# Kernel optimization log

Measured on AMD Instinct MI355X. Metric: run time of the kernel, lower is better.

Reference implementation:

```python
import jax, jax.numpy as jnp
import numpy as np

EPS = 1e-06
S = 0.025
ALPHA = 0.98
DELTA = 2.0
R = 0.5


def setup_inputs() -> dict:
    key = jax.random.key(0)
    # mel spectrogram magnitudes: non-negative
    x = jax.random.uniform(key, (32, 8192, 128), dtype=jnp.float32)
    return {"x": x}


def reference(x):
    # EMA smoother over time: M[0] = x[0]; M[t] = (1-s)*M[t-1] + s*x[t]
    # x: [B, T, F] -> scan over time with carry [B, F]
    def step(m_prev, x_t):
        m = (1.0 - S) * m_prev + S * x_t
        return m, m

    x_t_major = jnp.moveaxis(x[:, 1:, :], 1, 0)  # [T-1, B, F]
    _, ms = jax.lax.scan(step, x[:, 0, :], x_t_major)  # ms: [T-1, B, F]
    M = jnp.concatenate([x[:, :1, :], jnp.moveaxis(ms, 0, 1)], axis=1)  # [B, T, F]

    # PCEN: (x / (M + eps)^alpha + delta)^r - delta^r
    out = (x / jnp.power(M + EPS, ALPHA) + DELTA) ** R - DELTA ** R
    return out
```

## Files before the change

### kernel.cpp

```cpp
#include <hip/hip_runtime.h>
#include <math.h>


#define BB 32
#define TT 8192
#define FF 128
#define KK 64
#define CC (TT / KK)
#define WW 256
#define AA 0.975f
#define SS 0.025f

__device__ __forceinline__ float pcen_out(float xv, float m) {
    float mp = m + 1e-6f;
    float p = __builtin_amdgcn_exp2f(-0.98f * __builtin_amdgcn_logf(mp));
    return sqrtf(fmaf(xv, p, 2.0f)) - 1.41421356237309505f;
}

__global__ __launch_bounds__(128) void pcen_kernel(const float* __restrict__ x,
                                                   float* __restrict__ out) {
    const int job = blockIdx.x;
    const int b   = job >> 6;
    const int k   = job & (KK - 1);
    const int f   = threadIdx.x;
    const int t0  = k * CC;

    const size_t base = ((size_t)b * TT + t0) * FF + f;
    const float* xp = x + base;
    float*       op = out + base;

    float m;
    if (k == 0) {
        float xv = xp[0];
        m = xv;
        __builtin_nontemporal_store(pcen_out(xv, m), op);
    } else {
        const int w = (t0 < WW) ? t0 : WW;
        const float* wp = xp - (size_t)w * FF;
        m = wp[0];
        #pragma unroll 8
        for (int j = 1; j < w; ++j) {
            m = fmaf(AA, m, SS * wp[(size_t)j * FF]);
        }
        float xv = xp[0];
        m = fmaf(AA, m, SS * xv);
        __builtin_nontemporal_store(pcen_out(xv, m), op);
    }

    #pragma unroll 8
    for (int j = 1; j < CC; ++j) {
        float xv = xp[(size_t)j * FF];
        m = fmaf(AA, m, SS * xv);
        __builtin_nontemporal_store(pcen_out(xv, m), op + (size_t)j * FF);
    }
}

extern "C" void kernel_launch(void* const* d_in, const int* in_sizes, int n_in,
                              void* d_out, int out_size, void* d_ws, size_t ws_size,
                              hipStream_t stream) {
    const float* x = (const float*)d_in[0];
    float* out = (float*)d_out;
    (void)in_sizes; (void)n_in; (void)out_size; (void)d_ws; (void)ws_size;
    pcen_kernel<<<BB * KK, 128, 0, stream>>>(x, out);
}
```

Before: 83.93 us.

## Parallelize EMA scan within chunks using sub-group partial sums and float4 loads

Replaces the per-thread serial EMA over 128 timesteps plus a 256-step warmup window with a block-level two-level scan. Each 256-thread block handles 256 timesteps split into 8 groups of 32, and threads load float4 vectors. Groups compute local partial sums for the previous chunk (the warmup) and the current chunk, combine them through shared memory using the decay factor 0.975^32, and then each group rescans its 32 steps to write outputs. This shortens the serial dependency chain and raises memory parallelism. The cost is re-reading the input (warmup window and second pass) and a block barrier, and the truncated 256-step warmup is still an approximation of the full history.

```diff
diff --git a/kernel.cpp b/kernel.cpp
--- a/kernel.cpp
+++ b/kernel.cpp
@@ -5,53 +5,82 @@
 #define BB 32
 #define TT 8192
 #define FF 128
-#define KK 64
-#define CC (TT / KK)
-#define WW 256
+#define CC 256
+#define KK (TT / CC)
+#define GT 32
+#define NG (CC / GT)
+#define ST (FF / 4)
 #define AA 0.975f
 #define SS 0.025f
 
+using f32x4 = __attribute__((ext_vector_type(4))) float;
+
+constexpr float powf_n(float a, int n) {
+    float p = 1.0f;
+    for (int i = 0; i < n; ++i) p *= a;
+    return p;
+}
+constexpr float P32 = powf_n(0.975f, 32);
+
 __device__ __forceinline__ float pcen_out(float xv, float m) {
-    float mp = m + 1e-6f;
-    float p = __builtin_amdgcn_exp2f(-0.98f * __builtin_amdgcn_logf(mp));
+    float p = __builtin_amdgcn_exp2f(-0.98f * __builtin_amdgcn_logf(m + 1e-6f));
     return sqrtf(fmaf(xv, p, 2.0f)) - 1.41421356237309505f;
 }
 
-__global__ __launch_bounds__(128) void pcen_kernel(const float* __restrict__ x,
-                                                   float* __restrict__ out) {
-    const int job = blockIdx.x;
-    const int b   = job >> 6;
-    const int k   = job & (KK - 1);
-    const int f   = threadIdx.x;
+__global__ __launch_bounds__(256) void pcen_fused(const float* __restrict__ x,
+                                                  float* __restrict__ out) {
+    __shared__ f32x4 sW[NG][32];
+    __shared__ f32x4 sM[NG][32];
+    const int tid = threadIdx.x;
+    const int g   = tid >> 5;
+    const int f4  = tid & 31;
+    const int b   = blockIdx.x >> 5;
+    const int k   = blockIdx.x & (KK - 1);
     const int t0  = k * CC;
 
-    const size_t base = ((size_t)b * TT + t0) * FF + f;
-    const float* xp = x + base;
-    float*       op = out + base;
+    f32x4 sw = 0.0f;
+    if (k > 0) {
+        const f32x4* wp = (const f32x4*)(x + ((size_t)b * TT + (size_t)(t0 - CC)
+                                              + (size_t)g * GT) * FF) + f4;
+        f32x4 v0 = wp[0];
+        sw = (k == 1 && g == 0) ? v0 : SS * v0;
+        #pragma unroll
+        for (int i = 1; i < GT; ++i) sw = AA * sw + SS * wp[(size_t)i * ST];
+    }
+    sW[g][f4] = sw;
 
-    float m;
-    if (k == 0) {
-        float xv = xp[0];
-        m = xv;
-        __builtin_nontemporal_store(pcen_out(xv, m), op);
-    } else {
-        const int w = (t0 < WW) ? t0 : WW;
-        const float* wp = xp - (size_t)w * FF;
-        m = wp[0];
-        #pragma unroll 8
-        for (int j = 1; j < w; ++j) {
-            m = fmaf(AA, m, SS * wp[(size_t)j * FF]);
-        }
-        float xv = xp[0];
-        m = fmaf(AA, m, SS * xv);
-        __builtin_nontemporal_store(pcen_out(xv, m), op);
+    const f32x4* mp = (const f32x4*)(x + ((size_t)b * TT + (size_t)t0
+                                          + (size_t)g * GT) * FF) + f4;
+    {
+        f32x4 v0 = mp[0];
+        f32x4 sm = (k == 0 && g == 0) ? v0 : SS * v0;
+        #pragma unroll
+        for (int i = 1; i < GT; ++i) sm = AA * sm + SS * mp[(size_t)i * ST];
+        sM[g][f4] = sm;
     }
+    __syncthreads();
 
-    #pragma unroll 8
-    for (int j = 1; j < CC; ++j) {
-        float xv = xp[(size_t)j * FF];
-        m = fmaf(AA, m, SS * xv);
-        __builtin_nontemporal_store(pcen_out(xv, m), op + (size_t)j * FF);
+    f32x4 m = 0.0f;
+    if (k > 0) {
+        m = sW[0][f4];
+        #pragma unroll
+        for (int gg = 1; gg < NG; ++gg) m = P32 * m + sW[gg][f4];
+    }
+    for (int gg = 0; gg < g; ++gg) m = P32 * m + sM[gg][f4];
+
+    f32x4* op = (f32x4*)(out + ((size_t)b * TT + (size_t)t0
+                                + (size_t)g * GT) * FF) + f4;
+    #pragma unroll
+    for (int i = 0; i < GT; ++i) {
+        f32x4 v = mp[(size_t)i * ST];
+        if (i == 0 && k == 0 && g == 0) m = v;
+        else                            m = AA * m + SS * v;
+        f32x4 o;
+        o.x = pcen_out(v.x, m.x);
+        o.y = pcen_out(v.y, m.y);
+        o.z = pcen_out(v.z, m.z);
+        o.w = pcen_out(v.w, m.w);
+        __builtin_nontemporal_store(o, op + (size_t)i * ST);
     }
 }
 
@@ -61,5 +90,5 @@
     const float* x = (const float*)d_in[0];
     float* out = (float*)d_out;
     (void)in_sizes; (void)n_in; (void)out_size; (void)d_ws; (void)ws_size;
-    pcen_kernel<<<BB * KK, 128, 0, stream>>>(x, out);
+    pcen_fused<<<BB * KK, 256, 0, stream>>>(x, out);
 }
```

Result: no change. 84.03 us (+0.1%).
